# Kernel tuning notes

Hardware: AMD Instinct MI355X
Metric: run time of the kernel (lower is better)

## Reference

```python
import jax, jax.numpy as jnp
import numpy as np

B, N, H, W = 64, 32, 200, 200


def setup_inputs() -> dict:
    key = jax.random.key(0)
    k1, k2, k3, k4 = jax.random.split(key, 4)
    return {
        "parameter": jax.random.uniform(k1, (B, N, 3), dtype=jnp.float32),
        "x_start": jax.random.uniform(k2, (), dtype=jnp.float32),
        "y_start": jax.random.uniform(k3, (), dtype=jnp.float32),
        "theta": jax.random.uniform(k4, (), dtype=jnp.float32, minval=-3.14159, maxval=3.14159),
        # learned parameters at their torch init values
        "weights": jnp.eye(2, dtype=jnp.float32),
        "biases": jnp.zeros(2, dtype=jnp.float32),
        "thick_mult": jnp.array(0.5, dtype=jnp.float32),
        "thick_bias": jnp.array(0.1, dtype=jnp.float32),
        "dark_exp": jnp.array(1.0, dtype=jnp.float32),
        "dark_non_lin_weight": jnp.array(0.5, dtype=jnp.float32),
        "x_m": jnp.array(1.0, dtype=jnp.float32),
        "y_m": jnp.array(1.0, dtype=jnp.float32),
        "x_b": jnp.array(0.0, dtype=jnp.float32),
        "y_b": jnp.array(0.0, dtype=jnp.float32),
        "use_conv": 0,
    }


def reference(parameter, x_start, y_start, theta, weights, biases, thick_mult,
              thick_bias, dark_exp, dark_non_lin_weight, x_m, y_m, x_b, y_b,
              use_conv):
    # torch.flip(traj, dims=(2,)) then traj[:,:,0] *= -1:
    # channel0 (y) = -parameter[...,1], channel1 (x) = parameter[...,0]
    y0 = -parameter[..., 1]
    x0 = parameter[..., 0]
    # rotation about origin (vectorized over batch; identical per-element math)
    c, s = jnp.cos(theta), jnp.sin(theta)
    x_rot = x0 * c + y0 * s
    y_rot = -x0 * s + y0 * c
    yy = y_rot * y_m + y_b + y_start
    xx = x_rot * x_m + x_b + x_start
    traj = jnp.stack([yy, xx], axis=-1)                      # (B,N,2)
    # curve_to_stroke: matmul(weights, curve).T + biases == traj @ weights.T + biases
    strokes = traj @ weights.T + biases                      # (B,N,2)
    thick = (parameter[..., 2] * 2.0 + 0.5) / 64.0           # (B,N)
    # grid_coords: channel0 = row/H, channel1 = col/W
    gy = jnp.arange(H, dtype=strokes.dtype) / H
    gx = jnp.arange(W, dtype=strokes.dtype) / W
    coords = jnp.stack(jnp.meshgrid(gy, gx, indexing='ij'), axis=-1)  # (H,W,2)
    v = strokes[:, :-1, None, None, :]                       # (B,N-1,1,1,2)
    w = strokes[:, 1:, None, None, :]
    p = coords[None, None]                                   # (1,1,H,W,2)
    wv = w - v
    d2 = jnp.sum(wv * wv, axis=-1)                           # (B,N-1,1,1)
    dot = jnp.sum((p - v) * wv, axis=-1) / (d2 + 1e-5)       # (B,N-1,H,W)
    frac = jnp.clip(dot, 0.0, 1.0)
    proj = v + frac[..., None] * wv                          # (B,N-1,H,W,2)
    diff = p - proj
    dist = jnp.sqrt(jnp.sum(diff * diff, axis=-1))           # (B,N-1,H,W)
    th = thick[:, :-1, None, None] * (1.0 - frac) + thick[:, 1:, None, None] * frac
    th = jnp.maximum(th * thick_mult + thick_bias, 1e-8)
    dark = jnp.clip((th - dist) / th, 0.0, 1.0)
    dark = (dark + 1e-4) ** dark_exp
    nl = jax.nn.sigmoid(dark * 16.0 - 8.0)
    dark = dark_non_lin_weight * nl + (1.0 - dark_non_lin_weight) * dark
    return jnp.max(dark, axis=1)                             # (B,H,W)
```

## Files before the change

kernel.cpp:

```cpp
#include <hip/hip_runtime.h>
#include <math.h>

#define B_ 64
#define N_ 32
#define H_ 200
#define W_ 200
#define NSEG (N_ - 1)
#define TSX 32
#define TSY 16
#define NTX 7
#define NTY 13
#define TILE_RAD 0.087f

__global__ __launch_bounds__(128) void stroke_kernel(
    const float* __restrict__ param,
    const float* __restrict__ x_start,
    const float* __restrict__ y_start,
    const float* __restrict__ theta,
    const float* __restrict__ weights,
    const float* __restrict__ biases,
    const float* __restrict__ thick_mult,
    const float* __restrict__ thick_bias,
    const float* __restrict__ dark_exp_p,
    const float* __restrict__ dark_nlw_p,
    const float* __restrict__ x_m_p,
    const float* __restrict__ y_m_p,
    const float* __restrict__ x_b_p,
    const float* __restrict__ y_b_p,
    float* __restrict__ out)
{
    __shared__ float4 s_A[NSEG];
    __shared__ float4 s_B[NSEG];

    const int b    = blockIdx.z;
    const int tid  = threadIdx.x;
    const int lane = tid & 63;

    const float dexp = dark_exp_p[0], dnlw = dark_nlw_p[0];

    float sy = 0.0f, sx = 0.0f, tk = 0.0f;
    const float tm = thick_mult[0], tb = thick_bias[0];
    if (lane < N_) {
        const float thv = theta[0];
        const float c   = __cosf(thv), s = __sinf(thv);
        const float xs  = x_start[0], ys = y_start[0];
        const float W00 = weights[0], W01 = weights[1];
        const float W10 = weights[2], W11 = weights[3];
        const float bb0 = biases[0],  bb1 = biases[1];
        const float xm  = x_m_p[0], ym = y_m_p[0];
        const float xb  = x_b_p[0], yb = y_b_p[0];
        float p0 = param[(b * N_ + lane) * 3 + 0];
        float p1 = param[(b * N_ + lane) * 3 + 1];
        float p2 = param[(b * N_ + lane) * 3 + 2];
        float x0 = p0, y0 = -p1;
        float x_rot =  x0 * c + y0 * s;
        float y_rot = -x0 * s + y0 * c;
        float yy = y_rot * ym + yb + ys;
        float xx = x_rot * xm + xb + xs;
        sy = yy * W00 + xx * W01 + bb0;
        sx = yy * W10 + xx * W11 + bb1;
        tk = (p2 * 2.0f + 0.5f) * (1.0f / 64.0f);
    }
    float sy1 = __shfl_down(sy, 1);
    float sx1 = __shfl_down(sx, 1);
    float tk1 = __shfl_down(tk, 1);

    bool keep = false;
    float4 A4 = make_float4(0,0,0,0), B4 = make_float4(0,0,0,0);
    if (lane < NSEG) {
        float wvy = sy1 - sy, wvx = sx1 - sx;
        float d2 = wvy * wvy + wvx * wvx;
        float inv_d2 = 1.0f / (d2 + 1e-5f);
        float c0 = tk * tm + tb;
        float c1 = (tk1 - tk) * tm;
        A4 = make_float4(sy, sx, wvy, wvx);
        B4 = make_float4(inv_d2, c0, c1, wvx * inv_d2 * (1.0f / W_));
        const float cy = ((float)(blockIdx.y * TSY) + 7.5f)  * (1.0f / H_);
        const float cx = ((float)(blockIdx.x * TSX) + 15.5f) * (1.0f / W_);
        float dyc = cy - sy, dxc = cx - sx;
        float dot = (dyc * wvy + dxc * wvx) * inv_d2;
        float fr  = __builtin_amdgcn_fmed3f(dot, 0.0f, 1.0f);
        float ey  = dyc - fr * wvy;
        float ex  = dxc - fr * wvx;
        float e2c = ey * ey + ex * ex;
        float thmax = fmaxf(fmaxf(c0, c0 + c1), 1e-8f);
        float reach = thmax + TILE_RAD;
        keep = e2c < reach * reach;
    }
    unsigned long long mask = __ballot(keep);
    const int cnt = (int)__popcll(mask);
    if (keep) {
        int pos = (int)__popcll(mask & ((1ull << lane) - 1ull));
        s_A[pos] = A4; s_B[pos] = B4;
    }
    asm volatile("s_waitcnt lgkmcnt(0)" ::: "memory");

    const int ii = tid >> 3;
    const int jj = tid & 7;
    const int r  = blockIdx.y * TSY + ii;
    const int c0 = blockIdx.x * TSX + (jj << 2);
    const float py  = (float)r  * (1.0f / H_);
    const float px0 = (float)c0 * (1.0f / W_);

    const bool hoist = (dexp > 0.0f) && (dnlw >= 0.0f) && (dnlw <= 1.0f);

    float o0, o1, o2, o3;
    if (hoist) {
        float q0 = INFINITY, q1 = INFINITY, q2 = INFINITY, q3 = INFINITY;
        if (cnt > 0) {
            float4 A = s_A[0], Bc = s_B[0];
            for (int n = 0; n < cnt; ++n) {
                int np = (n + 1 < cnt) ? n + 1 : n;
                float4 An = s_A[np], Bn = s_B[np];
                float dy  = py  - A.x;
                float dx0 = px0 - A.y;
                float dx1 = dx0 + 1.0f / W_;
                float dx2 = dx0 + 2.0f / W_;
                float dx3 = dx0 + 3.0f / W_;
                float dot0 = fmaf(dy, A.z, dx0 * A.w) * Bc.x;
                float dot1 = dot0 + Bc.w;
                float dot2 = dot1 + Bc.w;
                float dot3 = dot2 + Bc.w;
                #define PX(dotv, dxv, qm) { \
                    float fr = __builtin_amdgcn_fmed3f(dotv, 0.0f, 1.0f); \
                    float ey = fmaf(-fr, A.z, dy); \
                    float ex = fmaf(-fr, A.w, dxv); \
                    float e2 = fmaf(ey, ey, ex * ex); \
                    float th = fmaxf(fmaf(fr, Bc.z, Bc.y), 1e-8f); \
                    float it = __builtin_amdgcn_rcpf(th); \
                    qm = fminf(qm, (e2 * it) * it); }
                PX(dot0, dx0, q0)
                PX(dot1, dx1, q1)
                PX(dot2, dx2, q2)
                PX(dot3, dx3, q3)
                #undef PX
                A = An; Bc = Bn;
            }
        }
        const bool lin = (dexp == 1.0f);
        #define EPI(qm, rr) { \
            float md = fminf(fmaxf(1.0f - __builtin_amdgcn_sqrtf(qm), 0.0f), 1.0f); \
            float d  = lin ? (md + 1e-4f) : __expf(dexp * __logf(md + 1e-4f)); \
            float nl = __builtin_amdgcn_rcpf(1.0f + __expf(8.0f - d * 16.0f)); \
            rr = dnlw * nl + (1.0f - dnlw) * d; }
        EPI(q0, o0) EPI(q1, o1) EPI(q2, o2) EPI(q3, o3)
        #undef EPI
    } else {
        float b0 = -INFINITY, b1 = -INFINITY, b2 = -INFINITY, b3 = -INFINITY;
        if (cnt < NSEG) {
            float d0  = __expf(dexp * __logf(1e-4f));
            float nl0 = __builtin_amdgcn_rcpf(1.0f + __expf(8.0f - d0 * 16.0f));
            float t0  = dnlw * nl0 + (1.0f - dnlw) * d0;
            b0 = b1 = b2 = b3 = t0;
        }
        for (int n = 0; n < cnt; ++n) {
            float4 A = s_A[n], Bc = s_B[n];
            float dy  = py  - A.x;
            float dx0 = px0 - A.y;
            float dx1 = dx0 + 1.0f / W_;
            float dx2 = dx0 + 2.0f / W_;
            float dx3 = dx0 + 3.0f / W_;
            float dot0 = fmaf(dy, A.z, dx0 * A.w) * Bc.x;
            float dot1 = dot0 + Bc.w;
            float dot2 = dot1 + Bc.w;
            float dot3 = dot2 + Bc.w;
            #define PXF(dotv, dxv, bb) { \
                float fr = __builtin_amdgcn_fmed3f(dotv, 0.0f, 1.0f); \
                float ey = fmaf(-fr, A.z, dy); \
                float ex = fmaf(-fr, A.w, dxv); \
                float dist = __builtin_amdgcn_sqrtf(fmaf(ey, ey, ex * ex)); \
                float th = fmaxf(fmaf(fr, Bc.z, Bc.y), 1e-8f); \
                float dark = fminf(fmaxf(fmaf(-dist, __builtin_amdgcn_rcpf(th), 1.0f), 0.0f), 1.0f); \
                float d  = __expf(dexp * __logf(dark + 1e-4f)); \
                float nl = __builtin_amdgcn_rcpf(1.0f + __expf(8.0f - d * 16.0f)); \
                bb = fmaxf(bb, dnlw * nl + (1.0f - dnlw) * d); }
            PXF(dot0, dx0, b0)
            PXF(dot1, dx1, b1)
            PXF(dot2, dx2, b2)
            PXF(dot3, dx3, b3)
            #undef PXF
        }
        o0 = b0; o1 = b1; o2 = b2; o3 = b3;
    }

    if (r < H_ && c0 < W_) {
        *reinterpret_cast<float4*>(&out[(b * H_ + r) * W_ + c0]) =
            make_float4(o0, o1, o2, o3);
    }
}

extern "C" void kernel_launch(void* const* d_in, const int* in_sizes, int n_in,
                              void* d_out, int out_size, void* d_ws, size_t ws_size,
                              hipStream_t stream) {
    const float* param      = (const float*)d_in[0];
    const float* x_start    = (const float*)d_in[1];
    const float* y_start    = (const float*)d_in[2];
    const float* theta      = (const float*)d_in[3];
    const float* weights    = (const float*)d_in[4];
    const float* biases     = (const float*)d_in[5];
    const float* thick_mult = (const float*)d_in[6];
    const float* thick_bias = (const float*)d_in[7];
    const float* dark_exp   = (const float*)d_in[8];
    const float* dark_nlw   = (const float*)d_in[9];
    const float* x_m        = (const float*)d_in[10];
    const float* y_m        = (const float*)d_in[11];
    const float* x_b        = (const float*)d_in[12];
    const float* y_b        = (const float*)d_in[13];
    float* out = (float*)d_out;

    dim3 block(128);
    dim3 grid(NTX, NTY, B_);
    stroke_kernel<<<grid, block, 0, stream>>>(
        param, x_start, y_start, theta, weights, biases,
        thick_mult, thick_bias, dark_exp, dark_nlw,
        x_m, y_m, x_b, y_b, out);
}
```

Baseline: 14.12 us.

## Split into cull and paint kernels with per-tile segment bitmasks in workspace

```diff
diff --git a/kernel.cpp b/kernel.cpp
--- a/kernel.cpp
+++ b/kernel.cpp
@@ -6,37 +6,33 @@
 #define H_ 200
 #define W_ 200
 #define NSEG (N_ - 1)
-#define TSX 32
-#define TSY 16
-#define NTX 7
-#define NTY 13
-#define TILE_RAD 0.087f
-
-__global__ __launch_bounds__(128) void stroke_kernel(
+
+#define TS2 16
+#define NT2 13
+#define NTILE (NT2 * NT2)
+#define TILE_RAD2 0.054f
+
+#define WS_MASK_BYTES (B_ * NTILE * 4)
+#define WS_SEGA_OFF   WS_MASK_BYTES
+#define WS_SEGA_BYTES (B_ * NSEG * 16)
+#define WS_SEGB_OFF   (WS_SEGA_OFF + WS_SEGA_BYTES)
+#define WS_NEEDED     (WS_SEGB_OFF + WS_SEGA_BYTES)
+
+__global__ __launch_bounds__(64) void cull_kernel(
     const float* __restrict__ param,
-    const float* __restrict__ x_start,
-    const float* __restrict__ y_start,
-    const float* __restrict__ theta,
-    const float* __restrict__ weights,
-    const float* __restrict__ biases,
-    const float* __restrict__ thick_mult,
+    const float* __restrict__ x_start,  const float* __restrict__ y_start,
+    const float* __restrict__ theta,    const float* __restrict__ weights,
+    const float* __restrict__ biases,   const float* __restrict__ thick_mult,
     const float* __restrict__ thick_bias,
-    const float* __restrict__ dark_exp_p,
-    const float* __restrict__ dark_nlw_p,
-    const float* __restrict__ x_m_p,
-    const float* __restrict__ y_m_p,
-    const float* __restrict__ x_b_p,
-    const float* __restrict__ y_b_p,
-    float* __restrict__ out)
+    const float* __restrict__ x_m_p,    const float* __restrict__ y_m_p,
+    const float* __restrict__ x_b_p,    const float* __restrict__ y_b_p,
+    unsigned* __restrict__ ws_mask,
+    float4*  __restrict__ ws_segA,
+    float4*  __restrict__ ws_segB)
 {
-    __shared__ float4 s_A[NSEG];
-    __shared__ float4 s_B[NSEG];
-
-    const int b    = blockIdx.z;
-    const int tid  = threadIdx.x;
-    const int lane = tid & 63;
-
-    const float dexp = dark_exp_p[0], dnlw = dark_nlw_p[0];
+    const int b    = blockIdx.y;
+    const int ty   = blockIdx.x;
+    const int lane = threadIdx.x;
 
     float sy = 0.0f, sx = 0.0f, tk = 0.0f;
     const float tm = thick_mult[0], tb = thick_bias[0];
@@ -65,6 +61,229 @@
     float sx1 = __shfl_down(sx, 1);
     float tk1 = __shfl_down(tk, 1);
 
+    const bool isseg = (lane < NSEG);
+    float wvy = 0, wvx = 0, inv_d2 = 0, c0 = 0, c1 = 0, thmax = 0;
+    if (isseg) {
+        wvy = sy1 - sy; wvx = sx1 - sx;
+        float d2 = wvy * wvy + wvx * wvx;
+        inv_d2 = 1.0f / (d2 + 1e-5f);
+        c0 = tk * tm + tb;
+        c1 = (tk1 - tk) * tm;
+        thmax = fmaxf(fmaxf(c0, c0 + c1), 1e-8f);
+        if (ty == 0) {
+            ws_segA[b * NSEG + lane] = make_float4(sy, sx, wvy, wvx);
+            ws_segB[b * NSEG + lane] =
+                make_float4(inv_d2, c0, c1, wvx * inv_d2 * (1.0f / W_));
+        }
+    }
+
+    const float segYmin = fminf(sy, sy1), segYmax = fmaxf(sy, sy1);
+    const float segXmin = fminf(sx, sx1), segXmax = fmaxf(sx, sx1);
+    const float reach   = thmax + TILE_RAD2;
+    const float reach2  = reach * reach;
+    const float th2     = thmax * thmax + 1e-7f;
+    const float cy   = ((float)(ty * TS2) + 7.5f) * (1.0f / H_);
+    const float tyLo = (float)(ty * TS2) * (1.0f / H_);
+    const float tyHi = (float)(ty * TS2 + (TS2 - 1)) * (1.0f / H_);
+    float gy = fmaxf(fmaxf(tyLo - segYmax, segYmin - tyHi), 0.0f);
+
+    for (int tx = 0; tx < NT2; ++tx) {
+        bool keep = false;
+        if (isseg) {
+            const float cx   = ((float)(tx * TS2) + 7.5f) * (1.0f / W_);
+            const float txLo = (float)(tx * TS2) * (1.0f / W_);
+            const float txHi = (float)(tx * TS2 + (TS2 - 1)) * (1.0f / W_);
+            float dyc = cy - sy, dxc = cx - sx;
+            float dot = (dyc * wvy + dxc * wvx) * inv_d2;
+            float fr  = __builtin_amdgcn_fmed3f(dot, 0.0f, 1.0f);
+            float ey  = dyc - fr * wvy;
+            float ex  = dxc - fr * wvx;
+            float e2c = ey * ey + ex * ex;
+            float gx = fmaxf(fmaxf(txLo - segXmax, segXmin - txHi), 0.0f);
+            keep = (e2c < reach2) && ((gx * gx + gy * gy) < th2);
+        }
+        unsigned mm = (unsigned)__ballot(keep);
+        if (lane == 0) ws_mask[(b * NT2 + ty) * NT2 + tx] = mm;
+    }
+}
+
+__global__ __launch_bounds__(256) void paint_kernel(
+    const float* __restrict__ dark_exp_p, const float* __restrict__ dark_nlw_p,
+    const unsigned* __restrict__ ws_mask,
+    const float4*  __restrict__ ws_segA,
+    const float4*  __restrict__ ws_segB,
+    float* __restrict__ out)
+{
+    __shared__ float4 sA_l[NSEG], sB_l[NSEG];
+
+    const int b   = blockIdx.y;
+    const int tid = threadIdx.x;
+
+    if (tid < 2 * NSEG) {
+        int s = tid >> 1;
+        if (tid & 1) sB_l[s] = ws_segB[b * NSEG + s];
+        else         sA_l[s] = ws_segA[b * NSEG + s];
+    }
+    __syncthreads();
+
+    const int t = blockIdx.x * 4 + (tid >> 6);
+    if (t >= NTILE) return;
+    const int lane = tid & 63;
+    const int ty = t / NT2, tx = t - ty * NT2;
+    const int r  = ty * TS2 + (lane >> 2);
+    const int c0 = tx * TS2 + ((lane & 3) << 2);
+    const float py  = (float)r  * (1.0f / H_);
+    const float px0 = (float)c0 * (1.0f / W_);
+
+    const unsigned mask = ws_mask[b * NTILE + t];
+    const float dexp = dark_exp_p[0], dnlw = dark_nlw_p[0];
+    const bool hoist = (dexp > 0.0f) && (dnlw >= 0.0f) && (dnlw <= 1.0f);
+
+    float o0, o1, o2, o3;
+    if (hoist) {
+        float q0 = INFINITY, q1 = INFINITY, q2 = INFINITY, q3 = INFINITY;
+        unsigned m = mask;
+        if (m) {
+            int s = __ffs(m) - 1;
+            float4 A = sA_l[s], Bc = sB_l[s];
+            for (;;) {
+                unsigned m2 = m & (m - 1u);
+                int sn = m2 ? (__ffs(m2) - 1) : 0;
+                float4 An = sA_l[sn], Bn = sB_l[sn];
+                float dy  = py  - A.x;
+                float dx0 = px0 - A.y;
+                float dx1 = dx0 + 1.0f / W_;
+                float dx2 = dx0 + 2.0f / W_;
+                float dx3 = dx0 + 3.0f / W_;
+                float dot0 = fmaf(dy, A.z, dx0 * A.w) * Bc.x;
+                float dot1 = dot0 + Bc.w;
+                float dot2 = dot1 + Bc.w;
+                float dot3 = dot2 + Bc.w;
+                #define PX(dotv, dxv, qm) { \
+                    float fr = __builtin_amdgcn_fmed3f(dotv, 0.0f, 1.0f); \
+                    float ey = fmaf(-fr, A.z, dy); \
+                    float ex = fmaf(-fr, A.w, dxv); \
+                    float e2 = fmaf(ey, ey, ex * ex); \
+                    float th = fmaxf(fmaf(fr, Bc.z, Bc.y), 1e-8f); \
+                    float it = __builtin_amdgcn_rcpf(th); \
+                    qm = fminf(qm, (e2 * it) * it); }
+                PX(dot0, dx0, q0)
+                PX(dot1, dx1, q1)
+                PX(dot2, dx2, q2)
+                PX(dot3, dx3, q3)
+                #undef PX
+                if (!m2) break;
+                m = m2; A = An; Bc = Bn;
+            }
+        }
+        const bool lin = (dexp == 1.0f);
+        #define EPI(qm, rr) { \
+            float md = fminf(fmaxf(1.0f - __builtin_amdgcn_sqrtf(qm), 0.0f), 1.0f); \
+            float d  = lin ? (md + 1e-4f) : __expf(dexp * __logf(md + 1e-4f)); \
+            float nl = __builtin_amdgcn_rcpf(1.0f + __expf(8.0f - d * 16.0f)); \
+            rr = dnlw * nl + (1.0f - dnlw) * d; }
+        EPI(q0, o0) EPI(q1, o1) EPI(q2, o2) EPI(q3, o3)
+        #undef EPI
+    } else {
+        float b0 = -INFINITY, b1 = -INFINITY, b2 = -INFINITY, b3 = -INFINITY;
+        if (__popc(mask) < NSEG) {
+            float d0  = __expf(dexp * __logf(1e-4f));
+            float nl0 = __builtin_amdgcn_rcpf(1.0f + __expf(8.0f - d0 * 16.0f));
+            float t0  = dnlw * nl0 + (1.0f - dnlw) * d0;
+            b0 = b1 = b2 = b3 = t0;
+        }
+        unsigned m = mask;
+        while (m) {
+            int s = __ffs(m) - 1;
+            m &= m - 1u;
+            float4 A = sA_l[s], Bc = sB_l[s];
+            float dy  = py  - A.x;
+            float dx0 = px0 - A.y;
+            float dx1 = dx0 + 1.0f / W_;
+            float dx2 = dx0 + 2.0f / W_;
+            float dx3 = dx0 + 3.0f / W_;
+            float dot0 = fmaf(dy, A.z, dx0 * A.w) * Bc.x;
+            float dot1 = dot0 + Bc.w;
+            float dot2 = dot1 + Bc.w;
+            float dot3 = dot2 + Bc.w;
+            #define PXF(dotv, dxv, bb) { \
+                float fr = __builtin_amdgcn_fmed3f(dotv, 0.0f, 1.0f); \
+                float ey = fmaf(-fr, A.z, dy); \
+                float ex = fmaf(-fr, A.w, dxv); \
+                float dist = __builtin_amdgcn_sqrtf(fmaf(ey, ey, ex * ex)); \
+                float th = fmaxf(fmaf(fr, Bc.z, Bc.y), 1e-8f); \
+                float dark = fminf(fmaxf(fmaf(-dist, __builtin_amdgcn_rcpf(th), 1.0f), 0.0f), 1.0f); \
+                float d  = __expf(dexp * __logf(dark + 1e-4f)); \
+                float nl = __builtin_amdgcn_rcpf(1.0f + __expf(8.0f - d * 16.0f)); \
+                bb = fmaxf(bb, dnlw * nl + (1.0f - dnlw) * d); }
+            PXF(dot0, dx0, b0)
+            PXF(dot1, dx1, b1)
+            PXF(dot2, dx2, b2)
+            PXF(dot3, dx3, b3)
+            #undef PXF
+        }
+        o0 = b0; o1 = b1; o2 = b2; o3 = b3;
+    }
+
+    if (r < H_ && c0 < W_) {
+        *reinterpret_cast<float4*>(&out[(b * H_ + r) * W_ + c0]) =
+            make_float4(o0, o1, o2, o3);
+    }
+}
+
+#define TSX 32
+#define TSY 16
+#define NTX 7
+#define NTY 13
+#define TILE_RAD 0.087f
+
+__global__ __launch_bounds__(128) void stroke_mono(
+    const float* __restrict__ param,
+    const float* __restrict__ x_start,  const float* __restrict__ y_start,
+    const float* __restrict__ theta,    const float* __restrict__ weights,
+    const float* __restrict__ biases,   const float* __restrict__ thick_mult,
+    const float* __restrict__ thick_bias,
+    const float* __restrict__ dark_exp_p, const float* __restrict__ dark_nlw_p,
+    const float* __restrict__ x_m_p,    const float* __restrict__ y_m_p,
+    const float* __restrict__ x_b_p,    const float* __restrict__ y_b_p,
+    float* __restrict__ out)
+{
+    __shared__ float4 s_A[NSEG];
+    __shared__ float4 s_B[NSEG];
+
+    const int b    = blockIdx.z;
+    const int tid  = threadIdx.x;
+    const int lane = tid & 63;
+
+    const float dexp = dark_exp_p[0], dnlw = dark_nlw_p[0];
+
+    float sy = 0.0f, sx = 0.0f, tk = 0.0f;
+    const float tm = thick_mult[0], tb = thick_bias[0];
+    if (lane < N_) {
+        const float thv = theta[0];
+        const float c   = __cosf(thv), s = __sinf(thv);
+        const float xs  = x_start[0], ys = y_start[0];
+        const float W00 = weights[0], W01 = weights[1];
+        const float W10 = weights[2], W11 = weights[3];
+        const float bb0 = biases[0],  bb1 = biases[1];
+        const float xm  = x_m_p[0], ym = y_m_p[0];
+        const float xb  = x_b_p[0], yb = y_b_p[0];
+        float p0 = param[(b * N_ + lane) * 3 + 0];
+        float p1 = param[(b * N_ + lane) * 3 + 1];
+        float p2 = param[(b * N_ + lane) * 3 + 2];
+        float x0 = p0, y0 = -p1;
+        float x_rot =  x0 * c + y0 * s;
+        float y_rot = -x0 * s + y0 * c;
+        float yy = y_rot * ym + yb + ys;
+        float xx = x_rot * xm + xb + xs;
+        sy = yy * W00 + xx * W01 + bb0;
+        sx = yy * W10 + xx * W11 + bb1;
+        tk = (p2 * 2.0f + 0.5f) * (1.0f / 64.0f);
+    }
+    float sy1 = __shfl_down(sy, 1);
+    float sx1 = __shfl_down(sx, 1);
+    float tk1 = __shfl_down(tk, 1);
+
     bool keep = false;
     float4 A4 = make_float4(0,0,0,0), B4 = make_float4(0,0,0,0);
     if (lane < NSEG) {
@@ -75,6 +294,7 @@
         float c1 = (tk1 - tk) * tm;
         A4 = make_float4(sy, sx, wvy, wvx);
         B4 = make_float4(inv_d2, c0, c1, wvx * inv_d2 * (1.0f / W_));
+        float thmax = fmaxf(fmaxf(c0, c0 + c1), 1e-8f);
         const float cy = ((float)(blockIdx.y * TSY) + 7.5f)  * (1.0f / H_);
         const float cx = ((float)(blockIdx.x * TSX) + 15.5f) * (1.0f / W_);
         float dyc = cy - sy, dxc = cx - sx;
@@ -83,7 +303,6 @@
         float ey  = dyc - fr * wvy;
         float ex  = dxc - fr * wvx;
         float e2c = ey * ey + ex * ex;
-        float thmax = fmaxf(fmaxf(c0, c0 + c1), 1e-8f);
         float reach = thmax + TILE_RAD;
         keep = e2c < reach * reach;
     }
@@ -208,10 +427,22 @@
     const float* y_b        = (const float*)d_in[13];
     float* out = (float*)d_out;
 
-    dim3 block(128);
-    dim3 grid(NTX, NTY, B_);
-    stroke_kernel<<<grid, block, 0, stream>>>(
-        param, x_start, y_start, theta, weights, biases,
-        thick_mult, thick_bias, dark_exp, dark_nlw,
-        x_m, y_m, x_b, y_b, out);
+    if (ws_size >= (size_t)WS_NEEDED) {
+        unsigned* ws_mask = (unsigned*)d_ws;
+        float4*   ws_segA = (float4*)((char*)d_ws + WS_SEGA_OFF);
+        float4*   ws_segB = (float4*)((char*)d_ws + WS_SEGB_OFF);
+
+        cull_kernel<<<dim3(NT2, B_), dim3(64), 0, stream>>>(
+            param, x_start, y_start, theta, weights, biases,
+            thick_mult, thick_bias, x_m, y_m, x_b, y_b,
+            ws_mask, ws_segA, ws_segB);
+
+        paint_kernel<<<dim3((NTILE + 3) / 4, B_), dim3(256), 0, stream>>>(
+            dark_exp, dark_nlw, ws_mask, ws_segA, ws_segB, out);
+    } else {
+        stroke_mono<<<dim3(NTX, NTY, B_), dim3(128), 0, stream>>>(
+            param, x_start, y_start, theta, weights, biases,
+            thick_mult, thick_bias, dark_exp, dark_nlw,
+            x_m, y_m, x_b, y_b, out);
+    }
 }
```

New measurement: 18.20 us. 28.9% more time.
